# Optimization experiments

Measured on AMD Instinct MI355X. Metric: run time of the kernel, lower is better.

## Reference

```python
import jax, jax.numpy as jnp
import numpy as np

B, N, QDIM = 2, 4096, 768
H, D = 8, 64  # num_head, head_dim; inner_dim = 512
INNER = H * D


def setup_inputs() -> dict:
    key = jax.random.key(0)
    ks = jax.random.split(key, 6)
    s = lambda fan_in: 1.0 / np.sqrt(fan_in)
    return {
        "x": jax.random.normal(ks[0], (B, N, QDIM), dtype=jnp.float32),
        "Wq": jax.random.normal(ks[1], (QDIM, INNER), dtype=jnp.float32) * s(QDIM),
        "Wk": jax.random.normal(ks[2], (QDIM, INNER), dtype=jnp.float32) * s(QDIM),
        "Wv": jax.random.normal(ks[3], (QDIM, INNER), dtype=jnp.float32) * s(QDIM),
        "Wout": jax.random.normal(ks[4], (INNER, QDIM), dtype=jnp.float32) * s(INNER),
        "b_out": jnp.zeros((QDIM,), dtype=jnp.float32),
    }


def reference(x, Wq, Wk, Wv, Wout, b_out):
    # x: [b, n, q_dim]; self-attention (kv = x), no mask, dropout = 0 (eval).
    scale = D ** -0.5
    # project and split heads: [b, n, h*d] -> [b, h, n, d]
    def heads(t):
        b, n, _ = t.shape
        return t.reshape(b, n, H, D).transpose(0, 2, 1, 3)
    q = heads(x @ Wq)
    k = heads(x @ Wk)
    v = heads(x @ Wv)
    qk = jnp.einsum("bhid,bhjd->bhij", q, k) * scale  # [b, h, n, n] -- O(n^2) matrix
    attn = jax.nn.softmax(qk, axis=-1)
    out = jnp.einsum("bhij,bhjd->bhid", attn, v)  # [b, h, n, d]
    out = out.transpose(0, 2, 1, 3).reshape(x.shape[0], x.shape[1], INNER)
    return out @ Wout + b_out
```

## Files before the change

### kernel.cpp

```cpp
#include <hip/hip_runtime.h>
#include <cstdint>
#include <cstddef>


typedef __attribute__((ext_vector_type(8))) short short8;
typedef __attribute__((ext_vector_type(4))) float f32x4;

__device__ __forceinline__ unsigned short f2bf(float f) {
  unsigned int u = __float_as_uint(f);
  u = (u + 0x7fffu + ((u >> 16) & 1u)) >> 16;
  return (unsigned short)u;
}

__device__ __forceinline__ float fast_exp2(float x) {
#if __has_builtin(__builtin_amdgcn_exp2f)
  return __builtin_amdgcn_exp2f(x);
#else
  return __expf(x * 0.69314718055994531f);
#endif
}

__device__ __forceinline__ void gld16(const void* g, void* l) {
  __builtin_amdgcn_global_load_lds(
      (__attribute__((address_space(1))) void*)const_cast<void*>(g),
      (__attribute__((address_space(3))) void*)l, 16, 0, 0);
}


__global__ __launch_bounds__(256) void cvt_x_k(const float* __restrict__ x,
                                               unsigned short* __restrict__ xb) {
  const size_t i = ((size_t)blockIdx.x * 256 + threadIdx.x) * 4;
  const float4 v = *(const float4*)(x + i);
  ushort4 u;
  u.x = f2bf(v.x); u.y = f2bf(v.y); u.z = f2bf(v.z); u.w = f2bf(v.w);
  *(ushort4*)(xb + i) = u;
}

__global__ __launch_bounds__(256) void transpose_w_k(
    const float* __restrict__ Wq, const float* __restrict__ Wk,
    const float* __restrict__ Wv, const float* __restrict__ Wout,
    unsigned short* __restrict__ Wt,
    unsigned short* __restrict__ WoT)
{
  __shared__ float t[32][33];
  const int z = blockIdx.z;
  const float* src = (z == 0) ? Wq : (z == 1) ? Wk : (z == 2) ? Wv : Wout;
  const int R = (z < 3) ? 768 : 512, C = (z < 3) ? 512 : 768;
  unsigned short* dst = (z < 3) ? (Wt + (size_t)z * 393216) : WoT;
  const int tx = threadIdx.x & 31, ty = threadIdx.x >> 5;
  const int c0 = blockIdx.x * 32, r0 = blockIdx.y * 32;
  if (c0 >= C || r0 >= R) return;
#pragma unroll
  for (int k = 0; k < 4; ++k)
    t[ty + 8 * k][tx] = src[(size_t)(r0 + ty + 8 * k) * C + c0 + tx];
  __syncthreads();
#pragma unroll
  for (int k = 0; k < 4; ++k)
    dst[(size_t)(c0 + ty + 8 * k) * R + r0 + tx] = f2bf(t[tx][ty + 8 * k]);
}


__global__ __launch_bounds__(256) void gemm_qkv_k(
    const unsigned short* __restrict__ A,
    const unsigned short* __restrict__ Wt,
    unsigned short* __restrict__ qb, unsigned short* __restrict__ kb,
    unsigned short* __restrict__ vtb) {
  __shared__ __align__(16) short Al[4096];
  __shared__ __align__(16) short Bl[4096];
  const int tid = threadIdx.x;
  const int w = tid >> 6, lane = tid & 63, quad = lane >> 4, l15 = lane & 15;
  const int wy = w >> 1, wx = w & 1;
  const int m0 = blockIdx.x * 128, n0 = blockIdx.y * 128;
  const int z = blockIdx.z;
  const unsigned short* Bt = Wt + (size_t)z * (512 * 768);

  f32x4 acc[4][4];
#pragma unroll
  for (int i = 0; i < 4; ++i)
#pragma unroll
    for (int j = 0; j < 4; ++j) acc[i][j] = (f32x4){0.f, 0.f, 0.f, 0.f};

  for (int k0 = 0; k0 < 768; k0 += 32) {
    __syncthreads();
#pragma unroll
    for (int s = 0; s < 2; ++s) {
      const int t = s * 256 + tid;
      gld16(A + (size_t)(m0 + (t >> 2)) * 768 + k0 + (t & 3) * 8,
            Al + s * 2048 + w * 512);
      gld16(Bt + (size_t)(n0 + (t >> 2)) * 768 + k0 + (t & 3) * 8,
            Bl + s * 2048 + w * 512);
    }
    __syncthreads();
    short8 af[4], bf[4];
#pragma unroll
    for (int i = 0; i < 4; ++i) {
      af[i] = *(const short8*)(Al + (wy * 64 + i * 16 + l15) * 32 + quad * 8);
      bf[i] = *(const short8*)(Bl + (wx * 64 + i * 16 + l15) * 32 + quad * 8);
    }
    if (z == 2) {
#pragma unroll
      for (int i = 0; i < 4; ++i)
#pragma unroll
        for (int j = 0; j < 4; ++j)
          acc[i][j] = __builtin_amdgcn_mfma_f32_16x16x32_bf16(af[i], bf[j], acc[i][j], 0, 0, 0);
    } else {
#pragma unroll
      for (int i = 0; i < 4; ++i)
#pragma unroll
        for (int j = 0; j < 4; ++j)
          acc[i][j] = __builtin_amdgcn_mfma_f32_16x16x32_bf16(bf[i], af[j], acc[i][j], 0, 0, 0);
    }
  }

  if (z == 2) {
#pragma unroll
    for (int i = 0; i < 4; ++i) {
#pragma unroll
      for (int j = 0; j < 4; ++j) {
        const int m0r = m0 + wy * 64 + i * 16 + quad * 4;
        const int n = n0 + wx * 64 + j * 16 + l15;
        const int b = m0r >> 12, nseq0 = m0r & 4095;
        const int h = n >> 6, d = n & 63;
        ushort4 u;
        u.x = f2bf(acc[i][j][0]); u.y = f2bf(acc[i][j][1]);
        u.z = f2bf(acc[i][j][2]); u.w = f2bf(acc[i][j][3]);
        *(ushort4*)(vtb + (size_t)((b * 8 + h) * 64 + d) * 4096 + nseq0) = u;
      }
    }
  } else {
    const float qs = 0.18033688011112042f;
#pragma unroll
    for (int i = 0; i < 4; ++i) {
#pragma unroll
      for (int j = 0; j < 4; ++j) {
        const int n0r = n0 + wx * 64 + i * 16 + quad * 4;
        const int m = m0 + wy * 64 + j * 16 + l15;
        const int b = m >> 12, nseq = m & 4095;
        const int h = n0r >> 6, d0 = n0r & 63;
        ushort4 u;
        if (z == 0) {
          u.x = f2bf(acc[i][j][0] * qs); u.y = f2bf(acc[i][j][1] * qs);
          u.z = f2bf(acc[i][j][2] * qs); u.w = f2bf(acc[i][j][3] * qs);
          *(ushort4*)(qb + (size_t)((b * 8 + h) * 4096 + nseq) * 64 + d0) = u;
        } else {
          u.x = f2bf(acc[i][j][0]); u.y = f2bf(acc[i][j][1]);
          u.z = f2bf(acc[i][j][2]); u.w = f2bf(acc[i][j][3]);
          *(ushort4*)(kb + (size_t)((b * 8 + h) * 4096 + nseq) * 64 + d0) = u;
        }
      }
    }
  }
}


__global__ __launch_bounds__(256) void attn_k(
    const unsigned short* __restrict__ qb,
    const unsigned short* __restrict__ kb,
    const unsigned short* __restrict__ vtb,
    unsigned short* __restrict__ ob) {
  __shared__ __align__(16) char smem[65536];
  short* Kl = (short*)smem;
  short* Vl = (short*)(smem + 16384);
  short* Pl = (short*)(smem + 32768);

  const int tid = threadIdx.x;
  const int w = tid >> 6, lane = tid & 63, quad = lane >> 4, l15 = lane & 15;
  const int g = w >> 1, wq = w & 1;
  const int bh = blockIdx.y;
  const int q0 = blockIdx.x * 128;
  const unsigned short* qbase = qb + (size_t)bh * 4096 * 64;
  const unsigned short* kbase = kb + (size_t)bh * 4096 * 64;
  const unsigned short* vbase = vtb + (size_t)bh * 64 * 4096;
  short* pw = Pl + w * 4096;
  short* KlG = Kl + g * 4096;
  short* VlG = Vl + g * 4096;
  const int jbase = g * 2048;
  const int e8 = l15 & 7;

  short8 qf[4][2];
#pragma unroll
  for (int qh = 0; qh < 4; ++qh) {
    const int qrow = q0 + wq * 64 + qh * 16 + l15;
    qf[qh][0] = *(const short8*)(qbase + (size_t)qrow * 64 + quad * 8);
    qf[qh][1] = *(const short8*)(qbase + (size_t)qrow * 64 + 32 + quad * 8);
  }

  const short one_bf = (short)0x3F80;
  const short8 vones = {one_bf, one_bf, one_bf, one_bf,
                        one_bf, one_bf, one_bf, one_bf};

  f32x4 Oacc[4][4];
#pragma unroll
  for (int qh = 0; qh < 4; ++qh)
#pragma unroll
    for (int nf = 0; nf < 4; ++nf) Oacc[qh][nf] = (f32x4){0.f, 0.f, 0.f, 0.f};
  f32x4 Lacc[4];
#pragma unroll
  for (int qh = 0; qh < 4; ++qh) Lacc[qh] = (f32x4){0.f, 0.f, 0.f, 0.f};

  for (int j0 = 0; j0 < 2048; j0 += 64) {
    const int jj = jbase + j0;
    __syncthreads();
#pragma unroll
    for (int c = 0; c < 2; ++c) {
#pragma unroll
      for (int hf = 0; hf < 2; ++hf) {
        const int row = wq * 32 + hf * 16;
        gld16(kbase + (size_t)(jj + row + (lane >> 2)) * 64 + c * 32 + (lane & 3) * 8,
              KlG + (c * 64 + row) * 32);
        gld16(vbase + (size_t)(row + (lane >> 2)) * 4096 + jj + c * 32 + (lane & 3) * 8,
              VlG + (c * 64 + row) * 32);
      }
    }
    __syncthreads();

#pragma unroll
    for (int kt = 0; kt < 4; ++kt) {
      const short8 ka0 = *(const short8*)(KlG + (0 * 64 + kt * 16 + l15) * 32 + quad * 8);
      const short8 ka1 = *(const short8*)(KlG + (1 * 64 + kt * 16 + l15) * 32 + quad * 8);
#pragma unroll
      for (int qh = 0; qh < 4; ++qh) {
        f32x4 st = (f32x4){0.f, 0.f, 0.f, 0.f};
        st = __builtin_amdgcn_mfma_f32_16x16x32_bf16(ka0, qf[qh][0], st, 0, 0, 0);
        st = __builtin_amdgcn_mfma_f32_16x16x32_bf16(ka1, qf[qh][1], st, 0, 0, 0);
        const unsigned int u0 = __float_as_uint(fast_exp2(st[0]));
        const unsigned int u1 = __float_as_uint(fast_exp2(st[1]));
        const unsigned int u2 = __float_as_uint(fast_exp2(st[2]));
        const unsigned int u3 = __float_as_uint(fast_exp2(st[3]));
        uint2 pd;
        pd.x = (u1 & 0xFFFF0000u) | (u0 >> 16);
        pd.y = (u3 & 0xFFFF0000u) | (u2 >> 16);
        *(uint2*)(pw + (qh * 16 + l15) * 64 +
                  (((2 * kt + (quad >> 1)) ^ e8) * 8 + (quad & 1) * 4)) = pd;
      }
    }

    asm volatile("s_waitcnt lgkmcnt(0)" ::: "memory");

#pragma unroll
    for (int c = 0; c < 2; ++c) {
      short8 pa[4];
#pragma unroll
      for (int qh = 0; qh < 4; ++qh)
        pa[qh] = *(const short8*)(pw + (qh * 16 + l15) * 64 +
                                  ((4 * c + quad) ^ e8) * 8);
#pragma unroll
      for (int nf = 0; nf < 4; ++nf) {
        const short8 vb = *(const short8*)(VlG + (c * 64 + nf * 16 + l15) * 32 + quad * 8);
#pragma unroll
        for (int qh = 0; qh < 4; ++qh)
          Oacc[qh][nf] = __builtin_amdgcn_mfma_f32_16x16x32_bf16(
              pa[qh], vb, Oacc[qh][nf], 0, 0, 0);
      }
#pragma unroll
      for (int qh = 0; qh < 4; ++qh)
        Lacc[qh] = __builtin_amdgcn_mfma_f32_16x16x32_bf16(pa[qh], vones, Lacc[qh], 0, 0, 0);
    }
  }

  __syncthreads();
  float* Ox = (float*)smem;
  float* Lx = (float*)(smem + 33280);
  if (g == 1) {
#pragma unroll
    for (int qh = 0; qh < 4; ++qh)
#pragma unroll
      for (int r = 0; r < 4; ++r) {
        const int rl = wq * 64 + qh * 16 + quad * 4 + r;
        Lx[rl] = Lacc[qh][r];
#pragma unroll
        for (int nf = 0; nf < 4; ++nf)
          Ox[rl * 65 + nf * 16 + l15] = Oacc[qh][nf][r];
      }
  }
  __syncthreads();
  if (g == 0) {
    const int b = bh >> 3, h = bh & 7;
#pragma unroll
    for (int qh = 0; qh < 4; ++qh)
#pragma unroll
      for (int r = 0; r < 4; ++r) {
        const int rl = wq * 64 + qh * 16 + quad * 4 + r;
        const float inv = 1.0f / (Lacc[qh][r] + Lx[rl]);
        const int row = q0 + rl;
#pragma unroll
        for (int nf = 0; nf < 4; ++nf)
          ob[(size_t)(b * 4096 + row) * 512 + h * 64 + nf * 16 + l15] =
              f2bf((Oacc[qh][nf][r] + Ox[rl * 65 + nf * 16 + l15]) * inv);
      }
  }
}


__global__ __launch_bounds__(256) void gemm_out_k(
    const unsigned short* __restrict__ A,
    const unsigned short* __restrict__ Bt,
    const float* __restrict__ bias, float* __restrict__ out) {
  __shared__ __align__(16) short Al[4096];
  __shared__ __align__(16) short Bl[2048];
  const int tid = threadIdx.x;
  const int w = tid >> 6, lane = tid & 63, quad = lane >> 4, l15 = lane & 15;
  const int m0 = blockIdx.x * 128, n0 = blockIdx.y * 64;

  f32x4 acc[2][4];
#pragma unroll
  for (int i = 0; i < 2; ++i)
#pragma unroll
    for (int j = 0; j < 4; ++j) acc[i][j] = (f32x4){0.f, 0.f, 0.f, 0.f};

  for (int k0 = 0; k0 < 512; k0 += 32) {
    __syncthreads();
#pragma unroll
    for (int s = 0; s < 2; ++s) {
      const int t = s * 256 + tid;
      gld16(A + (size_t)(m0 + (t >> 2)) * 512 + k0 + (t & 3) * 8,
            Al + s * 2048 + w * 512);
    }
    gld16(Bt + (size_t)(n0 + (tid >> 2)) * 512 + k0 + (tid & 3) * 8,
          Bl + w * 512);
    __syncthreads();
    short8 af[2], bf[4];
#pragma unroll
    for (int i = 0; i < 2; ++i)
      af[i] = *(const short8*)(Al + (w * 32 + i * 16 + l15) * 32 + quad * 8);
#pragma unroll
    for (int j = 0; j < 4; ++j)
      bf[j] = *(const short8*)(Bl + (j * 16 + l15) * 32 + quad * 8);
#pragma unroll
    for (int i = 0; i < 2; ++i)
#pragma unroll
      for (int j = 0; j < 4; ++j)
        acc[i][j] = __builtin_amdgcn_mfma_f32_16x16x32_bf16(bf[j], af[i], acc[i][j], 0, 0, 0);
  }

#pragma unroll
  for (int i = 0; i < 2; ++i) {
#pragma unroll
    for (int j = 0; j < 4; ++j) {
      const int col0 = n0 + j * 16 + quad * 4;
      const int m = m0 + w * 32 + i * 16 + l15;
      const float4 b4 = *(const float4*)(bias + col0);
      float4 o;
      o.x = acc[i][j][0] + b4.x; o.y = acc[i][j][1] + b4.y;
      o.z = acc[i][j][2] + b4.z; o.w = acc[i][j][3] + b4.w;
      *(float4*)(out + (size_t)m * 768 + col0) = o;
    }
  }
}


extern "C" void kernel_launch(void* const* d_in, const int* in_sizes, int n_in,
                              void* d_out, int out_size, void* d_ws, size_t ws_size,
                              hipStream_t stream) {
  const float* x    = (const float*)d_in[0];
  const float* Wq   = (const float*)d_in[1];
  const float* Wk   = (const float*)d_in[2];
  const float* Wv   = (const float*)d_in[3];
  const float* Wout = (const float*)d_in[4];
  const float* bout = (const float*)d_in[5];
  float* out = (float*)d_out;
  char* ws = (char*)d_ws;

  unsigned short* xb  = (unsigned short*)(ws);
  unsigned short* Wt  = (unsigned short*)(ws + 12582912);
  unsigned short* WoT = (unsigned short*)(ws + 14942208);
  unsigned short* qb  = (unsigned short*)(ws + 15728640);
  unsigned short* kb  = (unsigned short*)(ws + 24117248);
  unsigned short* vtb = (unsigned short*)(ws + 32505856);
  unsigned short* ob  = (unsigned short*)(ws + 40894464);

  cvt_x_k<<<6144, 256, 0, stream>>>(x, xb);
  transpose_w_k<<<dim3(24, 24, 4), 256, 0, stream>>>(Wq, Wk, Wv, Wout, Wt, WoT);
  gemm_qkv_k<<<dim3(64, 4, 3), 256, 0, stream>>>(xb, Wt, qb, kb, vtb);
  attn_k<<<dim3(32, 16), 256, 0, stream>>>(qb, kb, vtb, ob);
  gemm_out_k<<<dim3(64, 12), 256, 0, stream>>>(ob, WoT, bout, out);
}
```

Measured before the change: 240.7 us.

## Split attention KV range across two blocks and merge partial outputs

The attention kernel now splits the key range over a second grid dimension, so twice as many blocks run, each with half the key length and a smaller 32-key tile, which roughly halves the shared memory per block. Each split writes unnormalized bf16 partial outputs and row sums to reused workspace buffers, and a new merge kernel adds them and normalizes. The aim is more blocks in flight (512 to 1024) and higher occupancy on the many CUs. In exchange it adds an extra kernel launch, extra memory traffic for the partials, and an extra bf16 rounding of the unnormalized partial outputs. The shorter 32-key loop also means more barriers per key processed.

Measured after the change: 271.1 us. +12.7%, slower.

```diff
diff --git a/kernel.cpp b/kernel.cpp
--- a/kernel.cpp
+++ b/kernel.cpp
@@ -10,6 +10,10 @@
   unsigned int u = __float_as_uint(f);
   u = (u + 0x7fffu + ((u >> 16) & 1u)) >> 16;
   return (unsigned short)u;
+}
+
+__device__ __forceinline__ float bf2f(unsigned short u) {
+  return __uint_as_float((unsigned int)u << 16);
 }
 
 __device__ __forceinline__ float fast_exp2(float x) {
@@ -157,25 +161,28 @@
     const unsigned short* __restrict__ qb,
     const unsigned short* __restrict__ kb,
     const unsigned short* __restrict__ vtb,
-    unsigned short* __restrict__ ob) {
-  __shared__ __align__(16) char smem[65536];
+    unsigned short* __restrict__ op0,
+    unsigned short* __restrict__ op1,
+    float* __restrict__ lp) {
+  __shared__ __align__(16) char smem[33792];
   short* Kl = (short*)smem;
-  short* Vl = (short*)(smem + 16384);
-  short* Pl = (short*)(smem + 32768);
+  short* Vl = (short*)(smem + 8192);
+  short* Pl = (short*)(smem + 16384);
 
   const int tid = threadIdx.x;
   const int w = tid >> 6, lane = tid & 63, quad = lane >> 4, l15 = lane & 15;
   const int g = w >> 1, wq = w & 1;
+  const int z = blockIdx.z;
   const int bh = blockIdx.y;
   const int q0 = blockIdx.x * 128;
   const unsigned short* qbase = qb + (size_t)bh * 4096 * 64;
   const unsigned short* kbase = kb + (size_t)bh * 4096 * 64;
   const unsigned short* vbase = vtb + (size_t)bh * 64 * 4096;
-  short* pw = Pl + w * 4096;
-  short* KlG = Kl + g * 4096;
-  short* VlG = Vl + g * 4096;
-  const int jbase = g * 2048;
-  const int e8 = l15 & 7;
+  short* pw = Pl + w * 2048;
+  short* KlG = Kl + g * 2048;
+  short* VlG = Vl + g * 2048;
+  const int jbase = z * 2048 + g * 1024;
+  const int e4 = l15 & 3;
 
   short8 qf[4][2];
 #pragma unroll
@@ -198,26 +205,23 @@
 #pragma unroll
   for (int qh = 0; qh < 4; ++qh) Lacc[qh] = (f32x4){0.f, 0.f, 0.f, 0.f};
 
-  for (int j0 = 0; j0 < 2048; j0 += 64) {
+  for (int j0 = 0; j0 < 1024; j0 += 32) {
     const int jj = jbase + j0;
     __syncthreads();
 #pragma unroll
-    for (int c = 0; c < 2; ++c) {
-#pragma unroll
-      for (int hf = 0; hf < 2; ++hf) {
-        const int row = wq * 32 + hf * 16;
-        gld16(kbase + (size_t)(jj + row + (lane >> 2)) * 64 + c * 32 + (lane & 3) * 8,
-              KlG + (c * 64 + row) * 32);
-        gld16(vbase + (size_t)(row + (lane >> 2)) * 4096 + jj + c * 32 + (lane & 3) * 8,
-              VlG + (c * 64 + row) * 32);
-      }
-    }
-    __syncthreads();
-
-#pragma unroll
-    for (int kt = 0; kt < 4; ++kt) {
-      const short8 ka0 = *(const short8*)(KlG + (0 * 64 + kt * 16 + l15) * 32 + quad * 8);
-      const short8 ka1 = *(const short8*)(KlG + (1 * 64 + kt * 16 + l15) * 32 + quad * 8);
+    for (int c = 0; c < 2; ++c)
+      gld16(kbase + (size_t)(jj + wq * 16 + (lane >> 2)) * 64 + c * 32 + (lane & 3) * 8,
+            KlG + (c * 32 + wq * 16) * 32);
+#pragma unroll
+    for (int h16 = 0; h16 < 2; ++h16)
+      gld16(vbase + (size_t)(wq * 32 + h16 * 16 + (lane >> 2)) * 4096 + jj + (lane & 3) * 8,
+            VlG + (wq * 32 + h16 * 16) * 32);
+    __syncthreads();
+
+#pragma unroll
+    for (int kt = 0; kt < 2; ++kt) {
+      const short8 ka0 = *(const short8*)(KlG + (0 * 32 + kt * 16 + l15) * 32 + quad * 8);
+      const short8 ka1 = *(const short8*)(KlG + (1 * 32 + kt * 16 + l15) * 32 + quad * 8);
 #pragma unroll
       for (int qh = 0; qh < 4; ++qh) {
         f32x4 st = (f32x4){0.f, 0.f, 0.f, 0.f};
@@ -230,32 +234,28 @@
         uint2 pd;
         pd.x = (u1 & 0xFFFF0000u) | (u0 >> 16);
         pd.y = (u3 & 0xFFFF0000u) | (u2 >> 16);
-        *(uint2*)(pw + (qh * 16 + l15) * 64 +
-                  (((2 * kt + (quad >> 1)) ^ e8) * 8 + (quad & 1) * 4)) = pd;
+        *(uint2*)(pw + (qh * 16 + l15) * 32 +
+                  (((2 * kt + (quad >> 1)) ^ e4) * 8 + (quad & 1) * 4)) = pd;
       }
     }
 
     asm volatile("s_waitcnt lgkmcnt(0)" ::: "memory");
 
-#pragma unroll
-    for (int c = 0; c < 2; ++c) {
-      short8 pa[4];
+    short8 pa[4];
+#pragma unroll
+    for (int qh = 0; qh < 4; ++qh)
+      pa[qh] = *(const short8*)(pw + (qh * 16 + l15) * 32 + ((quad ^ e4) * 8));
+#pragma unroll
+    for (int nf = 0; nf < 4; ++nf) {
+      const short8 vb = *(const short8*)(VlG + (nf * 16 + l15) * 32 + quad * 8);
 #pragma unroll
       for (int qh = 0; qh < 4; ++qh)
-        pa[qh] = *(const short8*)(pw + (qh * 16 + l15) * 64 +
-                                  ((4 * c + quad) ^ e8) * 8);
-#pragma unroll
-      for (int nf = 0; nf < 4; ++nf) {
-        const short8 vb = *(const short8*)(VlG + (c * 64 + nf * 16 + l15) * 32 + quad * 8);
-#pragma unroll
-        for (int qh = 0; qh < 4; ++qh)
-          Oacc[qh][nf] = __builtin_amdgcn_mfma_f32_16x16x32_bf16(
-              pa[qh], vb, Oacc[qh][nf], 0, 0, 0);
-      }
-#pragma unroll
-      for (int qh = 0; qh < 4; ++qh)
-        Lacc[qh] = __builtin_amdgcn_mfma_f32_16x16x32_bf16(pa[qh], vones, Lacc[qh], 0, 0, 0);
-    }
+        Oacc[qh][nf] = __builtin_amdgcn_mfma_f32_16x16x32_bf16(
+            pa[qh], vb, Oacc[qh][nf], 0, 0, 0);
+    }
+#pragma unroll
+    for (int qh = 0; qh < 4; ++qh)
+      Lacc[qh] = __builtin_amdgcn_mfma_f32_16x16x32_bf16(pa[qh], vones, Lacc[qh], 0, 0, 0);
   }
 
   __syncthreads();
@@ -275,20 +275,42 @@
   }
   __syncthreads();
   if (g == 0) {
+    unsigned short* op = (z == 0) ? op0 : op1;
+    float* lz = lp + z * 65536 + bh * 4096;
     const int b = bh >> 3, h = bh & 7;
 #pragma unroll
     for (int qh = 0; qh < 4; ++qh)
 #pragma unroll
       for (int r = 0; r < 4; ++r) {
         const int rl = wq * 64 + qh * 16 + quad * 4 + r;
-        const float inv = 1.0f / (Lacc[qh][r] + Lx[rl]);
+        const float lsum = Lacc[qh][r] + Lx[rl];
+        if (l15 == 0) lz[q0 + rl] = lsum;
         const int row = q0 + rl;
 #pragma unroll
         for (int nf = 0; nf < 4; ++nf)
-          ob[(size_t)(b * 4096 + row) * 512 + h * 64 + nf * 16 + l15] =
-              f2bf((Oacc[qh][nf][r] + Ox[rl * 65 + nf * 16 + l15]) * inv);
+          op[(size_t)(b * 4096 + row) * 512 + h * 64 + nf * 16 + l15] =
+              f2bf(Oacc[qh][nf][r] + Ox[rl * 65 + nf * 16 + l15]);
       }
   }
+}
+
+
+__global__ __launch_bounds__(256) void merge_o_k(
+    const unsigned short* __restrict__ op0, const unsigned short* __restrict__ op1,
+    const float* __restrict__ lp, unsigned short* __restrict__ ob) {
+  const size_t i = ((size_t)blockIdx.x * 256 + threadIdx.x) * 4;
+  const int seq = (int)(i >> 9);
+  const int h = ((int)i & 511) >> 6;
+  const int lidx = ((seq >> 12) * 8 + h) * 4096 + (seq & 4095);
+  const float inv = 1.0f / (lp[lidx] + lp[65536 + lidx]);
+  const ushort4 p0 = *(const ushort4*)(op0 + i);
+  const ushort4 p1 = *(const ushort4*)(op1 + i);
+  ushort4 o;
+  o.x = f2bf((bf2f(p0.x) + bf2f(p1.x)) * inv);
+  o.y = f2bf((bf2f(p0.y) + bf2f(p1.y)) * inv);
+  o.z = f2bf((bf2f(p0.z) + bf2f(p1.z)) * inv);
+  o.w = f2bf((bf2f(p0.w) + bf2f(p1.w)) * inv);
+  *(ushort4*)(ob + i) = o;
 }
 
 
@@ -368,10 +390,14 @@
   unsigned short* kb  = (unsigned short*)(ws + 24117248);
   unsigned short* vtb = (unsigned short*)(ws + 32505856);
   unsigned short* ob  = (unsigned short*)(ws + 40894464);
+  unsigned short* op1 = xb;
+  float*          lpart = (float*)Wt;
+  unsigned short* op0 = ob;
 
   cvt_x_k<<<6144, 256, 0, stream>>>(x, xb);
   transpose_w_k<<<dim3(24, 24, 4), 256, 0, stream>>>(Wq, Wk, Wv, Wout, Wt, WoT);
   gemm_qkv_k<<<dim3(64, 4, 3), 256, 0, stream>>>(xb, Wt, qb, kb, vtb);
-  attn_k<<<dim3(32, 16), 256, 0, stream>>>(qb, kb, vtb, ob);
+  attn_k<<<dim3(32, 16, 2), 256, 0, stream>>>(qb, kb, vtb, op0, op1, lpart);
+  merge_o_k<<<4096, 256, 0, stream>>>(op0, op1, lpart, ob);
   gemm_out_k<<<dim3(64, 12), 256, 0, stream>>>(ob, WoT, bout, out);
 }
```
